# Performance work log

Hardware: AMD Instinct MI355X
Metric: run time of the kernel (lower is better)

## Reference

```python
import jax, jax.numpy as jnp
import numpy as np

N_NODES, NUM_GRAPHS, MAX_N = 65536, 512, 192
D, H = 512, 8
DH = D // H


def setup_inputs() -> dict:
    key = jax.random.key(0)
    ks = jax.random.split(key, 13)
    s = 1.0 / np.sqrt(D).astype(np.float32)
    return {
        "node_features": jax.random.normal(ks[0], (N_NODES, D), jnp.float32),
        "batch_indices": jnp.sort(jax.random.randint(ks[1], (N_NODES,), 0, NUM_GRAPHS)),
        "global_query": jax.random.normal(ks[2], (1, H, 1, DH), jnp.float32) * s,
        "w_q": jax.random.normal(ks[3], (D, D), jnp.float32) * s,
        "b_q": jax.random.normal(ks[4], (D,), jnp.float32) * 0.02,
        "w_k": jax.random.normal(ks[5], (D, D), jnp.float32) * s,
        "b_k": jax.random.normal(ks[6], (D,), jnp.float32) * 0.02,
        "w_v": jax.random.normal(ks[7], (D, D), jnp.float32) * s,
        "b_v": jax.random.normal(ks[8], (D,), jnp.float32) * 0.02,
        "w_o": jax.random.normal(ks[9], (D, D), jnp.float32) * s,
        "b_o": jax.random.normal(ks[10], (D,), jnp.float32) * 0.02,
        "w_p": jax.random.normal(ks[11], (D, D), jnp.float32) * s,
        "b_p": jax.random.normal(ks[12], (D,), jnp.float32) * 0.02,
    }


def reference(node_features, batch_indices, global_query, w_q, b_q, w_k, b_k,
              w_v, b_v, w_o, b_o, w_p, b_p):
    # ragged bookkeeping (batch_indices is sorted)
    counts = jax.ops.segment_sum(jnp.ones_like(batch_indices), batch_indices,
                                 num_segments=NUM_GRAPHS)            # [G]
    offsets = jnp.cumsum(counts) - counts                            # [G]
    pos = jnp.arange(N_NODES) - offsets[batch_indices]               # local node pos

    # pad nodes to dense [G, MAX_N, D]
    dense = jnp.zeros((NUM_GRAPHS, MAX_N, D), node_features.dtype)
    dense = dense.at[batch_indices, pos].set(node_features)
    mask = jnp.zeros((NUM_GRAPHS, MAX_N), bool).at[batch_indices, pos].set(True)

    # Faithful replication of torch's expand+reshape of global_query:
    # Q_in[g, t, d] = gq_flat[h*DH + d%DH] with h = (t*D + d) // (n_g*DH)
    gqf = global_query.reshape(H * DH)
    t = jnp.arange(MAX_N)[:, None]                                   # [MAX_N,1]
    d = jnp.arange(D)[None, :]                                       # [1,D]
    n = jnp.maximum(counts, 1)[:, None, None]                        # [G,1,1]
    h = jnp.clip((t * D + d)[None] // (n * DH), 0, H - 1)            # [G,MAX_N,D]
    q_in = gqf[h * DH + (d % DH)[None]]                              # [G,MAX_N,D]

    Q = (q_in @ w_q.T + b_q).reshape(NUM_GRAPHS, MAX_N, H, DH)
    K = (dense @ w_k.T + b_k).reshape(NUM_GRAPHS, MAX_N, H, DH)
    V = (dense @ w_v.T + b_v).reshape(NUM_GRAPHS, MAX_N, H, DH)

    scale = 1.0 / np.sqrt(DH).astype(np.float32)
    scores = jnp.einsum('gthd,gshd->ghts', Q, K) * scale             # [G,H,T,S]
    scores = jnp.where(mask[:, None, None, :], scores, -1e9)
    attn_w = jax.nn.softmax(scores, axis=-1)
    attn = jnp.einsum('ghts,gshd->gthd', attn_w, V).reshape(NUM_GRAPHS, MAX_N, D)
    attn = attn @ w_o.T + b_o

    denom = jnp.maximum(counts, 1).astype(attn.dtype)[:, None]
    pooled = (attn * mask[..., None].astype(attn.dtype)).sum(axis=1) / denom
    return jax.nn.relu(pooled @ w_p.T + b_p)                         # [G, D]
```

## Files before the change

### kernel.cpp

```cpp
#include <hip/hip_runtime.h>
#include <hip/hip_bf16.h>
#include <cstdint>

typedef __bf16 bf16;
typedef __attribute__((ext_vector_type(8))) __bf16 bf16x8;
typedef __attribute__((ext_vector_type(4))) __bf16 bf16x4;
typedef __attribute__((ext_vector_type(2))) __bf16 bf16x2;
typedef __attribute__((ext_vector_type(4))) float f32x4;

#define N_NODES    65536
#define NUM_GRAPHS 512
#define MAX_N      192
#define D          512
#define H          8
#define DH         64
#define UMAX       64
#define USTRIDE    132

__device__ __forceinline__ void gload_lds16(const void* g, void* l) {
    __builtin_amdgcn_global_load_lds((const __attribute__((address_space(1))) void*)g,
                                     (__attribute__((address_space(3))) void*)l, 16, 0, 0);
}

__global__ __launch_bounds__(256) void lb_kernel(const int* __restrict__ batch,
                                                 int* __restrict__ lb) {
    int g = blockIdx.x * 256 + threadIdx.x;
    if (g > NUM_GRAPHS) return;
    int lo = 0, hi = N_NODES;
    while (lo < hi) {
        int mid = (lo + hi) >> 1;
        if (batch[mid] < g) lo = mid + 1; else hi = mid;
    }
    lb[g] = lo;
}

__global__ __launch_bounds__(192) void dedup_kernel(const int* __restrict__ lb,
                                                    int* __restrict__ udata) {
    const int g = blockIdx.x;
    const int off = lb[g];
    const int n = min(lb[g + 1] - off, MAX_N);
    __shared__ int keys[MAX_N];
    const int t = threadIdx.x;
    if (t < n) {
        unsigned un = (unsigned)n;
        int key = 0;
        #pragma unroll
        for (int p = 0; p < 8; p++) key |= (int)(((unsigned)(8 * t + p)) / un) << (3 * p);
        keys[t] = key;
    }
    __syncthreads();
    if (t == 0) {
        int* base = udata + (size_t)g * USTRIDE;
        int nu = 0;
        for (int s = 0; s < n; s++) {
            if (s == 0 || keys[s] != keys[s - 1]) {
                if (nu < UMAX) { base[1 + nu] = keys[s]; base[65 + nu] = 0; nu++; }
            }
            base[65 + (nu - 1)] += 1;
        }
        base[0] = nu;
    }
}

__global__ __launch_bounds__(256) void cvt_kernel(const float* __restrict__ src,
                                                  bf16* __restrict__ dst, int n) {
    int i = (blockIdx.x * 256 + threadIdx.x) * 4;
    if (i >= n) return;
    float4 v = *(const float4*)(src + i);
    bf16x4 o = {(bf16)v.x, (bf16)v.y, (bf16)v.z, (bf16)v.w};
    *(bf16x4*)(dst + i) = o;
}

__global__ __launch_bounds__(256) void p2_kernel(const float* __restrict__ gq,
                                                 const float* __restrict__ wq,
                                                 float* __restrict__ P2) {
    int h = blockIdx.x, p = blockIdx.y;
    __shared__ float gs[64];
    if (threadIdx.x < 64) gs[threadIdx.x] = gq[h * 64 + threadIdx.x];
    __syncthreads();
    for (int o = threadIdx.x; o < D; o += 256) {
        const float* wr = wq + (size_t)o * D + p * 64;
        float acc = 0.f;
        #pragma unroll 16
        for (int j = 0; j < 64; j++) acc += gs[j] * wr[j];
        P2[(size_t)(h * 8 + p) * D + o] = acc;
    }
}

__global__ __launch_bounds__(256) void wov_kernel(const float* __restrict__ wo,
                                                  const float* __restrict__ wv,
                                                  bf16* __restrict__ Wov) {
    const int ot = blockIdx.x;
    const int h  = blockIdx.y;
    __shared__ float wos[32 * 64];
    for (int idx = threadIdx.x; idx < 32 * 64; idx += 256) {
        int ol = idx >> 6, j = idx & 63;
        wos[idx] = wo[(size_t)(ot * 32 + ol) * D + h * 64 + j];
    }
    __syncthreads();
    const int c = threadIdx.x * 2;
    float acc0[32] = {}, acc1[32] = {};
    for (int j = 0; j < 64; j++) {
        float2 v2 = *(const float2*)(wv + (size_t)(h * 64 + j) * D + c);
        #pragma unroll
        for (int o = 0; o < 32; o++) {
            float wj = wos[o * 64 + j];
            acc0[o] += wj * v2.x; acc1[o] += wj * v2.y;
        }
    }
    #pragma unroll
    for (int o = 0; o < 32; o++) {
        bf16x2 r = {(bf16)acc0[o], (bf16)acc1[o]};
        *(bf16x2*)(Wov + (size_t)(ot * 32 + o) * 4096 + h * 512 + c) = r;
    }
}

__global__ __launch_bounds__(256) void cst_kernel(const float* __restrict__ wo,
                                                  const float* __restrict__ bv,
                                                  const float* __restrict__ bo,
                                                  float* __restrict__ cst) {
    int o = blockIdx.x * 256 + threadIdx.x;
    if (o >= D) return;
    const float* wr = wo + (size_t)o * D;
    float acc = bo[o];
    for (int d0 = 0; d0 < D; d0 += 4) {
        float4 wv4 = *(const float4*)(wr + d0);
        float4 b4  = *(const float4*)(bv + d0);
        acc += wv4.x * b4.x + wv4.y * b4.y + wv4.z * b4.z + wv4.w * b4.w;
    }
    cst[o] = acc;
}

__global__ __launch_bounds__(256) void k_gemm(const float* __restrict__ Af,
                                              const bf16* __restrict__ Wkb,
                                              const float* __restrict__ bkb,
                                              bf16* __restrict__ Kout) {
    const int lin = blockIdx.x;
    const int xcd = lin & 7;
    const int idx = lin >> 3;
    const int nt  = idx & 3;
    const int ml  = idx >> 2;
    const int i0 = (xcd * 64 + ml) * 128;
    const int o0 = nt * 128;

    __shared__ char smem[20480];
    bf16* As = (bf16*)smem;
    bf16* Bs = (bf16*)(smem + 10240);
    const int tid = threadIdx.x;
    const int lane = tid & 63;
    const int w = tid >> 6;
    const int wm = w & 1, wn = w >> 1;
    const int fr = lane & 15, quad = lane >> 4;
    const int sr = lane >> 2;
    const int sc = (lane & 3) * 8;
    const float* gA = Af + (size_t)(i0 + w * 32 + sr) * D + sc;
    const bf16*  gB = Wkb + (size_t)(o0 + w * 32 + sr) * D + sc;
    bf16* lA = As + (w * 32 + sr) * 40 + sc;
    bf16* lB = Bs + (w * 32 + sr) * 40 + sc;

    f32x4 acc[4][4] = {};

    float4 a0 = *(const float4*)(gA);
    float4 a1 = *(const float4*)(gA + 4);
    float4 a2 = *(const float4*)(gA + (size_t)16 * D);
    float4 a3 = *(const float4*)(gA + (size_t)16 * D + 4);
    bf16x8 pb0 = *(const bf16x8*)(gB);
    bf16x8 pb1 = *(const bf16x8*)(gB + (size_t)16 * D);

    for (int kt = 0; kt < D; kt += 32) {
        __syncthreads();
        bf16x8 wA0 = {(bf16)a0.x,(bf16)a0.y,(bf16)a0.z,(bf16)a0.w,
                      (bf16)a1.x,(bf16)a1.y,(bf16)a1.z,(bf16)a1.w};
        bf16x8 wA1 = {(bf16)a2.x,(bf16)a2.y,(bf16)a2.z,(bf16)a2.w,
                      (bf16)a3.x,(bf16)a3.y,(bf16)a3.z,(bf16)a3.w};
        *(bf16x8*)lA = wA0;
        *(bf16x8*)(lA + 16 * 40) = wA1;
        *(bf16x8*)lB = pb0;
        *(bf16x8*)(lB + 16 * 40) = pb1;
        __syncthreads();
        bf16x8 fa[4], fb[4];
        #pragma unroll
        for (int mf = 0; mf < 4; mf++)
            fa[mf] = *(const bf16x8*)(As + (wm * 64 + mf * 16 + fr) * 40 + quad * 8);
        #pragma unroll
        for (int nf = 0; nf < 4; nf++)
            fb[nf] = *(const bf16x8*)(Bs + (wn * 64 + nf * 16 + fr) * 40 + quad * 8);
        if (kt + 32 < D) {
            a0 = *(const float4*)(gA + kt + 32);
            a1 = *(const float4*)(gA + kt + 36);
            a2 = *(const float4*)(gA + (size_t)16 * D + kt + 32);
            a3 = *(const float4*)(gA + (size_t)16 * D + kt + 36);
            pb0 = *(const bf16x8*)(gB + kt + 32);
            pb1 = *(const bf16x8*)(gB + (size_t)16 * D + kt + 32);
        }
        #pragma unroll
        for (int mf = 0; mf < 4; mf++)
            #pragma unroll
            for (int nf = 0; nf < 4; nf++)
                acc[mf][nf] = __builtin_amdgcn_mfma_f32_16x16x32_bf16(fa[mf], fb[nf], acc[mf][nf], 0, 0, 0);
    }

    bf16* Cs = (bf16*)smem;
    #pragma unroll
    for (int pass = 0; pass < 2; pass++) {
        __syncthreads();
        if (wm == pass) {
            #pragma unroll
            for (int nf = 0; nf < 4; nf++) {
                const int col = wn * 64 + nf * 16 + fr;
                const float bs = bkb[o0 + col];
                #pragma unroll
                for (int mf = 0; mf < 4; mf++) {
                    #pragma unroll
                    for (int r = 0; r < 4; r++)
                        Cs[(mf * 16 + quad * 4 + r) * 132 + col] = (bf16)(acc[mf][nf][r] + bs);
                }
            }
        }
        __syncthreads();
        #pragma unroll
        for (int k = 0; k < 4; k++) {
            int idx2 = k * 256 + tid;
            int row = idx2 >> 4;
            int coff = (idx2 & 15) * 8;
            bf16x8 v = *(const bf16x8*)(Cs + row * 132 + coff);
            *(bf16x8*)(Kout + (size_t)(i0 + pass * 64 + row) * D + o0 + coff) = v;
        }
    }
}

__global__ __launch_bounds__(512) void attn_kernel(const bf16* __restrict__ Kb,
                                                   const float* __restrict__ P2,
                                                   const float* __restrict__ bq,
                                                   const int* __restrict__ lb,
                                                   const int* __restrict__ udata,
                                                   const float* __restrict__ Af,
                                                   bf16* __restrict__ abar) {
    const int g = blockIdx.x;
    const int tid = threadIdx.x;
    const int lane = tid & 63;
    const int w = tid >> 6;
    const int h = w;
    const int off = lb[g];
    const int n = min(lb[g + 1] - off, MAX_N);

    __shared__ bf16 Qs[8][16 * 80];
    __shared__ float wacc[8][MAX_N];
    __shared__ int upat_l[UMAX], ucnt_l[UMAX];

    bf16* outg = abar + (size_t)g * 4096;
    if (n == 0) {
        const bf16 z0 = (bf16)0.f;
        bf16x8 z = {z0, z0, z0, z0, z0, z0, z0, z0};
        *(bf16x8*)(outg + tid * 8) = z;
        return;
    }

    const int* ubase = udata + (size_t)g * USTRIDE;
    const int nu = ubase[0];
    if (tid < 64) {
        upat_l[tid] = (tid < nu) ? ubase[1 + tid] : 0;
        ucnt_l[tid] = (tid < nu) ? ubase[65 + tid] : 0;
    }
    wacc[w][lane] = 0.f; wacc[w][64 + lane] = 0.f; wacc[w][128 + lane] = 0.f;
    __syncthreads();

    const int fr = lane & 15;
    const int quad = lane >> 4;
    const float inv_n = 1.0f / (float)n;

    for (int c0 = 0; c0 < nu; c0 += 16) {
        {
            const int ul = lane >> 2;
            const int j0 = (lane & 3) * 16;
            const bool valid = (c0 + ul) < nu;
            const int pat = upat_l[c0 + ul];
            const float* bpq = bq + h * 64 + j0;
            float4 q0 = *(const float4*)bpq;
            float4 q1 = *(const float4*)(bpq + 4);
            float4 q2 = *(const float4*)(bpq + 8);
            float4 q3 = *(const float4*)(bpq + 12);
            #pragma unroll
            for (int p = 0; p < 8; p++) {
                const int hp = (pat >> (3 * p)) & 7;
                const float* pp = P2 + (size_t)(hp * 8 + p) * D + h * 64 + j0;
                float4 t0 = *(const float4*)pp;
                float4 t1 = *(const float4*)(pp + 4);
                float4 t2 = *(const float4*)(pp + 8);
                float4 t3 = *(const float4*)(pp + 12);
                q0.x += t0.x; q0.y += t0.y; q0.z += t0.z; q0.w += t0.w;
                q1.x += t1.x; q1.y += t1.y; q1.z += t1.z; q1.w += t1.w;
                q2.x += t2.x; q2.y += t2.y; q2.z += t2.z; q2.w += t2.w;
                q3.x += t3.x; q3.y += t3.y; q3.z += t3.z; q3.w += t3.w;
            }
            if (!valid) {
                q0.x=q0.y=q0.z=q0.w=0.f; q1.x=q1.y=q1.z=q1.w=0.f;
                q2.x=q2.y=q2.z=q2.w=0.f; q3.x=q3.y=q3.z=q3.w=0.f;
            }
            bf16x8 b0 = {(bf16)q0.x,(bf16)q0.y,(bf16)q0.z,(bf16)q0.w,
                         (bf16)q1.x,(bf16)q1.y,(bf16)q1.z,(bf16)q1.w};
            bf16x8 b1 = {(bf16)q2.x,(bf16)q2.y,(bf16)q2.z,(bf16)q2.w,
                         (bf16)q3.x,(bf16)q3.y,(bf16)q3.z,(bf16)q3.w};
            *(bf16x8*)(&Qs[w][ul * 80 + j0])     = b0;
            *(bf16x8*)(&Qs[w][ul * 80 + j0 + 8]) = b1;
        }
        bf16x8 fa0 = *(const bf16x8*)(&Qs[w][fr * 80 + quad * 8]);
        bf16x8 fa1 = *(const bf16x8*)(&Qs[w][fr * 80 + 32 + quad * 8]);

        f32x4 sc[12];
        #pragma unroll
        for (int st = 0; st < 12; st++) {
            if (st * 16 < n) {
                int s = st * 16 + fr;
                int row = off + (s < n ? s : n - 1);
                const bf16* kp = Kb + (size_t)row * D + h * 64 + quad * 8;
                bf16x8 fb0 = *(const bf16x8*)kp;
                bf16x8 fb1 = *(const bf16x8*)(kp + 32);
                f32x4 a = {0.f, 0.f, 0.f, 0.f};
                a = __builtin_amdgcn_mfma_f32_16x16x32_bf16(fa0, fb0, a, 0, 0, 0);
                a = __builtin_amdgcn_mfma_f32_16x16x32_bf16(fa1, fb1, a, 0, 0, 0);
                if (s < n) {
                    sc[st].x = a.x * 0.125f; sc[st].y = a.y * 0.125f;
                    sc[st].z = a.z * 0.125f; sc[st].w = a.w * 0.125f;
                } else {
                    sc[st].x = sc[st].y = sc[st].z = sc[st].w = -1e30f;
                }
            } else {
                sc[st].x = sc[st].y = sc[st].z = sc[st].w = -1e30f;
            }
        }
        float m[4] = {-1e30f, -1e30f, -1e30f, -1e30f};
        #pragma unroll
        for (int st = 0; st < 12; st++) {
            m[0] = fmaxf(m[0], sc[st].x); m[1] = fmaxf(m[1], sc[st].y);
            m[2] = fmaxf(m[2], sc[st].z); m[3] = fmaxf(m[3], sc[st].w);
        }
        #pragma unroll
        for (int o = 1; o <= 8; o <<= 1) {
            #pragma unroll
            for (int r = 0; r < 4; r++) m[r] = fmaxf(m[r], __shfl_xor(m[r], o));
        }
        float den[4] = {0.f, 0.f, 0.f, 0.f};
        #pragma unroll
        for (int st = 0; st < 12; st++) {
            float e0 = __expf(sc[st].x - m[0]); float e1 = __expf(sc[st].y - m[1]);
            float e2 = __expf(sc[st].z - m[2]); float e3 = __expf(sc[st].w - m[3]);
            sc[st].x = e0; sc[st].y = e1; sc[st].z = e2; sc[st].w = e3;
            den[0] += e0; den[1] += e1; den[2] += e2; den[3] += e3;
        }
        #pragma unroll
        for (int o = 1; o <= 8; o <<= 1) {
            #pragma unroll
            for (int r = 0; r < 4; r++) den[r] += __shfl_xor(den[r], o);
        }
        float wf[4];
        #pragma unroll
        for (int r = 0; r < 4; r++)
            wf[r] = (float)ucnt_l[c0 + quad * 4 + r] * inv_n / den[r];
        #pragma unroll
        for (int st = 0; st < 12; st++) {
            float v = sc[st].x * wf[0] + sc[st].y * wf[1] + sc[st].z * wf[2] + sc[st].w * wf[3];
            v += __shfl_xor(v, 16);
            v += __shfl_xor(v, 32);
            if (lane < 16) wacc[w][st * 16 + lane] += v;
        }
    }

    __syncthreads();
    const float* Ac = Af + (size_t)off * D + tid;
    float accv[8] = {};
    for (int s = 0; s < n; s++) {
        float av = Ac[(size_t)s * D];
        #pragma unroll
        for (int hh = 0; hh < 8; hh++) accv[hh] += wacc[hh][s] * av;
    }
    #pragma unroll
    for (int hh = 0; hh < 8; hh++) outg[hh * 512 + tid] = (bf16)accv[hh];
}

__global__ __launch_bounds__(256) void zero_kernel(float* __restrict__ p, int n4) {
    int i = blockIdx.x * 256 + threadIdx.x;
    if (i < n4) { float4 z = {0.f, 0.f, 0.f, 0.f}; *(float4*)(p + i * 4) = z; }
}

__global__ __launch_bounds__(256) void og_gemm(const bf16* __restrict__ Ab,
                                               const bf16* __restrict__ Bb,
                                               float* __restrict__ Yt) {
    const int o0 = blockIdx.x * 128;
    const int i0 = blockIdx.y * 128;
    const int k0 = blockIdx.z * 512;
    __shared__ bf16 As[128 * 32];
    __shared__ bf16 Bs[128 * 32];
    const int tid = threadIdx.x;
    const int lane = tid & 63;
    const int w = tid >> 6;
    const int wm = w & 1, wn = w >> 1;
    const int fr = lane & 15, quad = lane >> 4;
    const bf16* gA = Ab + (size_t)(i0 + w * 32 + (lane >> 2)) * 4096 + k0 + (lane & 3) * 8;
    const bf16* gB = Bb + (size_t)(o0 + w * 32 + (lane >> 2)) * 4096 + k0 + (lane & 3) * 8;
    bf16* lA = As + (w * 32) * 32;
    bf16* lB = Bs + (w * 32) * 32;

    f32x4 acc[4][4] = {};

    for (int kt = 0; kt < 512; kt += 32) {
        __syncthreads();
        gload_lds16(gA + kt, lA);
        gload_lds16(gA + (size_t)16 * 4096 + kt, lA + 16 * 32);
        gload_lds16(gB + kt, lB);
        gload_lds16(gB + (size_t)16 * 4096 + kt, lB + 16 * 32);
        __syncthreads();
        bf16x8 fa[4], fb[4];
        #pragma unroll
        for (int mf = 0; mf < 4; mf++)
            fa[mf] = *(const bf16x8*)(As + (wm * 64 + mf * 16 + fr) * 32 + quad * 8);
        #pragma unroll
        for (int nf = 0; nf < 4; nf++)
            fb[nf] = *(const bf16x8*)(Bs + (wn * 64 + nf * 16 + fr) * 32 + quad * 8);
        #pragma unroll
        for (int mf = 0; mf < 4; mf++)
            #pragma unroll
            for (int nf = 0; nf < 4; nf++)
                acc[mf][nf] = __builtin_amdgcn_mfma_f32_16x16x32_bf16(fa[mf], fb[nf], acc[mf][nf], 0, 0, 0);
    }
    #pragma unroll
    for (int nf = 0; nf < 4; nf++) {
        const int col = o0 + wn * 64 + nf * 16 + fr;
        #pragma unroll
        for (int mf = 0; mf < 4; mf++) {
            const int row = i0 + wm * 64 + mf * 16 + quad * 4;
            #pragma unroll
            for (int r = 0; r < 4; r++)
                atomicAdd(&Yt[(size_t)(row + r) * D + col], acc[mf][nf][r]);
        }
    }
}

__global__ __launch_bounds__(256) void proj_p(const float* __restrict__ tmp,
                                              const float* __restrict__ cst,
                                              const bf16* __restrict__ Wpb,
                                              const float* __restrict__ bp,
                                              const int* __restrict__ lb,
                                              float* __restrict__ out) {
    const int o0 = blockIdx.x * 128;
    const int i0 = blockIdx.y * 128;
    __shared__ bf16 As[128 * 32];
    __shared__ bf16 Bs[128 * 32];
    const int tid = threadIdx.x;
    const int lane = tid & 63;
    const int w = tid >> 6;
    const int wm = w & 1, wn = w >> 1;
    const int fr = lane & 15, quad = lane >> 4;
    const int ar = tid >> 1;
    const int ac = (tid & 1) * 16;
    const int g = i0 + ar;
    const bool live = lb[g + 1] - lb[g] > 0;
    const float* tp = tmp + (size_t)g * D + ac;
    const float* cp = cst + ac;
    const bf16* gB = Wpb + (size_t)(o0 + w * 32 + (lane >> 2)) * D + (lane & 3) * 8;
    bf16* lB = Bs + (w * 32) * 32;

    f32x4 acc[4][4] = {};

    for (int kt = 0; kt < D; kt += 32) {
        __syncthreads();
        gload_lds16(gB + kt, lB);
        gload_lds16(gB + (size_t)16 * D + kt, lB + 16 * 32);
        {
            float4 x0 = *(const float4*)(tp + kt);
            float4 x1 = *(const float4*)(tp + kt + 4);
            float4 x2 = *(const float4*)(tp + kt + 8);
            float4 x3 = *(const float4*)(tp + kt + 12);
            float4 c0 = *(const float4*)(cp + kt);
            float4 c1 = *(const float4*)(cp + kt + 4);
            float4 c2 = *(const float4*)(cp + kt + 8);
            float4 c3 = *(const float4*)(cp + kt + 12);
            float s = live ? 1.f : 0.f;
            bf16x8 v0 = {(bf16)((x0.x+c0.x)*s),(bf16)((x0.y+c0.y)*s),(bf16)((x0.z+c0.z)*s),(bf16)((x0.w+c0.w)*s),
                         (bf16)((x1.x+c1.x)*s),(bf16)((x1.y+c1.y)*s),(bf16)((x1.z+c1.z)*s),(bf16)((x1.w+c1.w)*s)};
            bf16x8 v1 = {(bf16)((x2.x+c2.x)*s),(bf16)((x2.y+c2.y)*s),(bf16)((x2.z+c2.z)*s),(bf16)((x2.w+c2.w)*s),
                         (bf16)((x3.x+c3.x)*s),(bf16)((x3.y+c3.y)*s),(bf16)((x3.z+c3.z)*s),(bf16)((x3.w+c3.w)*s)};
            *(bf16x8*)(As + ar * 32 + ac) = v0;
            *(bf16x8*)(As + ar * 32 + ac + 8) = v1;
        }
        __syncthreads();
        bf16x8 fa[4], fb[4];
        #pragma unroll
        for (int mf = 0; mf < 4; mf++)
            fa[mf] = *(const bf16x8*)(As + (wm * 64 + mf * 16 + fr) * 32 + quad * 8);
        #pragma unroll
        for (int nf = 0; nf < 4; nf++)
            fb[nf] = *(const bf16x8*)(Bs + (wn * 64 + nf * 16 + fr) * 32 + quad * 8);
        #pragma unroll
        for (int mf = 0; mf < 4; mf++)
            #pragma unroll
            for (int nf = 0; nf < 4; nf++)
                acc[mf][nf] = __builtin_amdgcn_mfma_f32_16x16x32_bf16(fa[mf], fb[nf], acc[mf][nf], 0, 0, 0);
    }
    #pragma unroll
    for (int nf = 0; nf < 4; nf++) {
        const int col = o0 + wn * 64 + nf * 16 + fr;
        const float bs = bp[col];
        #pragma unroll
        for (int mf = 0; mf < 4; mf++) {
            const int row = i0 + wm * 64 + mf * 16 + quad * 4;
            #pragma unroll
            for (int r = 0; r < 4; r++)
                out[(size_t)(row + r) * D + col] = fmaxf(acc[mf][nf][r] + bs, 0.f);
        }
    }
}

extern "C" void kernel_launch(void* const* d_in, const int* in_sizes, int n_in,
                              void* d_out, int out_size, void* d_ws, size_t ws_size,
                              hipStream_t stream) {
    const float* nf    = (const float*)d_in[0];
    const int*   batch = (const int*)d_in[1];
    const float* gq    = (const float*)d_in[2];
    const float* wq    = (const float*)d_in[3];
    const float* bq    = (const float*)d_in[4];
    const float* wk    = (const float*)d_in[5];
    const float* bk    = (const float*)d_in[6];
    const float* wv    = (const float*)d_in[7];
    const float* bv    = (const float*)d_in[8];
    const float* wo    = (const float*)d_in[9];
    const float* bo    = (const float*)d_in[10];
    const float* wp    = (const float*)d_in[11];
    const float* bp    = (const float*)d_in[12];
    float* out = (float*)d_out;

    char* ws = (char*)d_ws;
    bf16*  abar = (bf16*)(ws + ((size_t)2 << 20));
    bf16*  Wov  = (bf16*)(ws + ((size_t)6 << 20));
    float* tmp  = (float*)(ws + ((size_t)10 << 20));
    float* cst  = (float*)(ws + ((size_t)11 << 20));
    bf16*  Kb   = (bf16*)(ws + ((size_t)64 << 20));
    char* sm = ws + ((size_t)128 << 20);
    int*  lb    = (int*)sm;    sm += 4096;
    int*  udata = (int*)sm;    sm += (size_t)NUM_GRAPHS * USTRIDE * 4 + 2048;
    bf16* Wkb   = (bf16*)sm;   sm += (size_t)D * D * 2;
    bf16* Wpb   = (bf16*)sm;   sm += (size_t)D * D * 2;
    float* P2   = (float*)sm;  sm += (size_t)64 * D * 4;

    lb_kernel<<<3, 256, 0, stream>>>(batch, lb);
    dedup_kernel<<<NUM_GRAPHS, 192, 0, stream>>>(lb, udata);
    cvt_kernel<<<(D * D / 4) / 256, 256, 0, stream>>>(wk, Wkb, D * D);
    cvt_kernel<<<(D * D / 4) / 256, 256, 0, stream>>>(wp, Wpb, D * D);
    p2_kernel<<<dim3(8, 8), 256, 0, stream>>>(gq, wq, P2);
    k_gemm<<<2048, 256, 0, stream>>>(nf, Wkb, bk, Kb);
    wov_kernel<<<dim3(16, 8), 256, 0, stream>>>(wo, wv, Wov);
    cst_kernel<<<2, 256, 0, stream>>>(wo, bv, bo, cst);
    attn_kernel<<<NUM_GRAPHS, 512, 0, stream>>>(Kb, P2, bq, lb, udata, nf, abar);
    zero_kernel<<<(NUM_GRAPHS * D / 4 + 255) / 256, 256, 0, stream>>>(tmp, NUM_GRAPHS * D / 4);
    og_gemm<<<dim3(4, 4, 8), 256, 0, stream>>>(abar, Wov, tmp);
    proj_p<<<dim3(4, 4), 256, 0, stream>>>(tmp, cst, Wpb, bp, lb, out);
}
```

Before: 436.6 us.

## Pre-convert node features to bf16, use direct-to-LDS loads, hoist K fragments

Node features are converted to bf16 in a separate pass into workspace. The K-projection GEMM then fills shared memory with global_load_lds instead of converting fp32 in registers. That drops the padded LDS layout and the register prefetch of the next tile. The attention kernel loads each head's K fragments into registers once, before the chunk loop, instead of reloading them every iteration. The dedup kernel now stages its results in shared memory and writes them out in parallel. In exchange there is an extra full read and write pass over the node features, possible LDS bank conflicts from the unpadded stride, no prefetch overlap, and higher register pressure in the attention kernel.

```diff
diff --git a/kernel.cpp b/kernel.cpp
--- a/kernel.cpp
+++ b/kernel.cpp
@@ -40,6 +40,8 @@
     const int off = lb[g];
     const int n = min(lb[g + 1] - off, MAX_N);
     __shared__ int keys[MAX_N];
+    __shared__ int ukey[UMAX], ucnt[UMAX];
+    __shared__ int nu_s;
     const int t = threadIdx.x;
     if (t < n) {
         unsigned un = (unsigned)n;
@@ -50,16 +52,20 @@
     }
     __syncthreads();
     if (t == 0) {
-        int* base = udata + (size_t)g * USTRIDE;
         int nu = 0;
         for (int s = 0; s < n; s++) {
             if (s == 0 || keys[s] != keys[s - 1]) {
-                if (nu < UMAX) { base[1 + nu] = keys[s]; base[65 + nu] = 0; nu++; }
+                if (nu < UMAX) { ukey[nu] = keys[s]; ucnt[nu] = 0; nu++; }
             }
-            base[65 + (nu - 1)] += 1;
-        }
-        base[0] = nu;
-    }
+            ucnt[nu - 1] += 1;
+        }
+        nu_s = nu;
+    }
+    __syncthreads();
+    const int nu = nu_s;
+    int* base = udata + (size_t)g * USTRIDE;
+    if (t == 0) base[0] = nu;
+    if (t < nu) { base[1 + t] = ukey[t]; base[65 + t] = ucnt[t]; }
 }
 
 __global__ __launch_bounds__(256) void cvt_kernel(const float* __restrict__ src,
@@ -131,7 +137,7 @@
     cst[o] = acc;
 }
 
-__global__ __launch_bounds__(256) void k_gemm(const float* __restrict__ Af,
+__global__ __launch_bounds__(256) void k_gemm(const bf16* __restrict__ Ab,
                                               const bf16* __restrict__ Wkb,
                                               const float* __restrict__ bkb,
                                               bf16* __restrict__ Kout) {
@@ -143,56 +149,35 @@
     const int i0 = (xcd * 64 + ml) * 128;
     const int o0 = nt * 128;
 
-    __shared__ char smem[20480];
+    __shared__ char smem[16896];
     bf16* As = (bf16*)smem;
-    bf16* Bs = (bf16*)(smem + 10240);
+    bf16* Bs = (bf16*)(smem + 8192);
     const int tid = threadIdx.x;
     const int lane = tid & 63;
     const int w = tid >> 6;
     const int wm = w & 1, wn = w >> 1;
     const int fr = lane & 15, quad = lane >> 4;
-    const int sr = lane >> 2;
-    const int sc = (lane & 3) * 8;
-    const float* gA = Af + (size_t)(i0 + w * 32 + sr) * D + sc;
-    const bf16*  gB = Wkb + (size_t)(o0 + w * 32 + sr) * D + sc;
-    bf16* lA = As + (w * 32 + sr) * 40 + sc;
-    bf16* lB = Bs + (w * 32 + sr) * 40 + sc;
+    const bf16* gA = Ab + (size_t)(i0 + w * 32 + (lane >> 2)) * D + (lane & 3) * 8;
+    const bf16* gB = Wkb + (size_t)(o0 + w * 32 + (lane >> 2)) * D + (lane & 3) * 8;
+    bf16* lA = As + (w * 32) * 32;
+    bf16* lB = Bs + (w * 32) * 32;
 
     f32x4 acc[4][4] = {};
 
-    float4 a0 = *(const float4*)(gA);
-    float4 a1 = *(const float4*)(gA + 4);
-    float4 a2 = *(const float4*)(gA + (size_t)16 * D);
-    float4 a3 = *(const float4*)(gA + (size_t)16 * D + 4);
-    bf16x8 pb0 = *(const bf16x8*)(gB);
-    bf16x8 pb1 = *(const bf16x8*)(gB + (size_t)16 * D);
-
     for (int kt = 0; kt < D; kt += 32) {
         __syncthreads();
-        bf16x8 wA0 = {(bf16)a0.x,(bf16)a0.y,(bf16)a0.z,(bf16)a0.w,
-                      (bf16)a1.x,(bf16)a1.y,(bf16)a1.z,(bf16)a1.w};
-        bf16x8 wA1 = {(bf16)a2.x,(bf16)a2.y,(bf16)a2.z,(bf16)a2.w,
-                      (bf16)a3.x,(bf16)a3.y,(bf16)a3.z,(bf16)a3.w};
-        *(bf16x8*)lA = wA0;
-        *(bf16x8*)(lA + 16 * 40) = wA1;
-        *(bf16x8*)lB = pb0;
-        *(bf16x8*)(lB + 16 * 40) = pb1;
+        gload_lds16(gA + kt, lA);
+        gload_lds16(gA + (size_t)16 * D + kt, lA + 16 * 32);
+        gload_lds16(gB + kt, lB);
+        gload_lds16(gB + (size_t)16 * D + kt, lB + 16 * 32);
         __syncthreads();
         bf16x8 fa[4], fb[4];
         #pragma unroll
         for (int mf = 0; mf < 4; mf++)
-            fa[mf] = *(const bf16x8*)(As + (wm * 64 + mf * 16 + fr) * 40 + quad * 8);
+            fa[mf] = *(const bf16x8*)(As + (wm * 64 + mf * 16 + fr) * 32 + quad * 8);
         #pragma unroll
         for (int nf = 0; nf < 4; nf++)
-            fb[nf] = *(const bf16x8*)(Bs + (wn * 64 + nf * 16 + fr) * 40 + quad * 8);
-        if (kt + 32 < D) {
-            a0 = *(const float4*)(gA + kt + 32);
-            a1 = *(const float4*)(gA + kt + 36);
-            a2 = *(const float4*)(gA + (size_t)16 * D + kt + 32);
-            a3 = *(const float4*)(gA + (size_t)16 * D + kt + 36);
-            pb0 = *(const bf16x8*)(gB + kt + 32);
-            pb1 = *(const bf16x8*)(gB + (size_t)16 * D + kt + 32);
-        }
+            fb[nf] = *(const bf16x8*)(Bs + (wn * 64 + nf * 16 + fr) * 32 + quad * 8);
         #pragma unroll
         for (int mf = 0; mf < 4; mf++)
             #pragma unroll
@@ -268,6 +253,16 @@
     const int fr = lane & 15;
     const int quad = lane >> 4;
     const float inv_n = 1.0f / (float)n;
+
+    bf16x8 kf0[12], kf1[12];
+    #pragma unroll
+    for (int st = 0; st < 12; st++) {
+        int s = st * 16 + fr;
+        int row = off + (s < n ? s : n - 1);
+        const bf16* kp = Kb + (size_t)row * D + h * 64 + quad * 8;
+        kf0[st] = *(const bf16x8*)kp;
+        kf1[st] = *(const bf16x8*)(kp + 32);
+    }
 
     for (int c0 = 0; c0 < nu; c0 += 16) {
         {
@@ -312,13 +307,9 @@
         for (int st = 0; st < 12; st++) {
             if (st * 16 < n) {
                 int s = st * 16 + fr;
-                int row = off + (s < n ? s : n - 1);
-                const bf16* kp = Kb + (size_t)row * D + h * 64 + quad * 8;
-                bf16x8 fb0 = *(const bf16x8*)kp;
-                bf16x8 fb1 = *(const bf16x8*)(kp + 32);
                 f32x4 a = {0.f, 0.f, 0.f, 0.f};
-                a = __builtin_amdgcn_mfma_f32_16x16x32_bf16(fa0, fb0, a, 0, 0, 0);
-                a = __builtin_amdgcn_mfma_f32_16x16x32_bf16(fa1, fb1, a, 0, 0, 0);
+                a = __builtin_amdgcn_mfma_f32_16x16x32_bf16(fa0, kf0[st], a, 0, 0, 0);
+                a = __builtin_amdgcn_mfma_f32_16x16x32_bf16(fa1, kf1[st], a, 0, 0, 0);
                 if (s < n) {
                     sc[st].x = a.x * 0.125f; sc[st].y = a.y * 0.125f;
                     sc[st].z = a.z * 0.125f; sc[st].w = a.w * 0.125f;
@@ -530,6 +521,7 @@
     float* out = (float*)d_out;
 
     char* ws = (char*)d_ws;
+    bf16*  Abf  = (bf16*)ws;
     bf16*  abar = (bf16*)(ws + ((size_t)2 << 20));
     bf16*  Wov  = (bf16*)(ws + ((size_t)6 << 20));
     float* tmp  = (float*)(ws + ((size_t)10 << 20));
@@ -547,7 +539,8 @@
     cvt_kernel<<<(D * D / 4) / 256, 256, 0, stream>>>(wk, Wkb, D * D);
     cvt_kernel<<<(D * D / 4) / 256, 256, 0, stream>>>(wp, Wpb, D * D);
     p2_kernel<<<dim3(8, 8), 256, 0, stream>>>(gq, wq, P2);
-    k_gemm<<<2048, 256, 0, stream>>>(nf, Wkb, bk, Kb);
+    cvt_kernel<<<(N_NODES * D / 4) / 256, 256, 0, stream>>>(nf, Abf, N_NODES * D);
+    k_gemm<<<2048, 256, 0, stream>>>(Abf, Wkb, bk, Kb);
     wov_kernel<<<dim3(16, 8), 256, 0, stream>>>(wo, wv, Wov);
     cst_kernel<<<2, 256, 0, stream>>>(wo, bv, bo, cst);
     attn_kernel<<<NUM_GRAPHS, 512, 0, stream>>>(Kb, P2, bq, lb, udata, nf, abar);
```

Result: slower. 449.6 us (+3.0%).
